# Performance work log

Measured on AMD Instinct MI355X. Metric: run time of the kernel, lower is better.

The kernel has to match this reference:

```python
import jax, jax.numpy as jnp
import numpy as np

LN_EPS = 1e-3  # keras LayerNormalization default epsilon


def setup_inputs() -> dict:
    key = jax.random.key(0)
    ks = jax.random.split(key, 6)
    B, S, D, H, K = 4, 4096, 1024, 16, 64
    scale = 1.0 / np.sqrt(D)
    return {
        "x": jax.random.normal(ks[0], (B, S, D), jnp.float32),
        "Wq": jax.random.normal(ks[1], (D, H, K), jnp.float32) * scale,
        "bq": jnp.zeros((H, K), jnp.float32),
        "Wk": jax.random.normal(ks[2], (D, H, K), jnp.float32) * scale,
        "bk": jnp.zeros((H, K), jnp.float32),
        "Wv": jax.random.normal(ks[3], (D, H, K), jnp.float32) * scale,
        "bv": jnp.zeros((H, K), jnp.float32),
        "Wo": jax.random.normal(ks[4], (H, K, D), jnp.float32) * scale,
        "bo": jnp.zeros((D,), jnp.float32),
        "gamma": jnp.ones((D,), jnp.float32),
        "beta": jnp.zeros((D,), jnp.float32),
        "num_window": 8,
    }


def reference(x, Wq, bq, Wk, bk, Wv, bv, Wo, bo, gamma, beta, num_window):
    B, S, D = x.shape
    H, K = Wq.shape[1], Wq.shape[2]
    Sw = S // num_window
    # Block-diagonal (windowed) attention: reshape seq into windows instead of a Python loop.
    xw = x.reshape(B, num_window, Sw, D)  # [B, W, Sw, D]
    q = jnp.einsum('bwsd,dhk->bwshk', xw, Wq) + bq
    k = jnp.einsum('bwsd,dhk->bwshk', xw, Wk) + bk
    v = jnp.einsum('bwsd,dhk->bwshk', xw, Wv) + bv
    scores = jnp.einsum('bwqhk,bwshk->bwhqs', q, k) / jnp.sqrt(jnp.asarray(K, x.dtype))
    attn = jax.nn.softmax(scores, axis=-1)  # [B, W, H, Sw, Sw]
    ctx = jnp.einsum('bwhqs,bwshk->bwqhk', attn, v)
    attn_out = (jnp.einsum('bwqhk,hkd->bwqd', ctx, Wo) + bo).reshape(B, S, D)
    # residual + layernorm (keras eps=1e-3)
    y = x + attn_out
    mu = jnp.mean(y, axis=-1, keepdims=True)
    var = jnp.mean(jnp.square(y - mu), axis=-1, keepdims=True)
    return (y - mu) * jax.lax.rsqrt(var + LN_EPS) * gamma + beta
```

## Files before the change

### kernel.cpp

```cpp
#include <hip/hip_runtime.h>

typedef __bf16 bf16_t;
typedef __bf16 bf16x4 __attribute__((ext_vector_type(4)));
typedef __bf16 bf16x8 __attribute__((ext_vector_type(8)));
typedef float f32x4 __attribute__((ext_vector_type(4)));

#define MFMA16(a, b, c) __builtin_amdgcn_mfma_f32_16x16x32_bf16((a), (b), (c), 0, 0, 0)

__device__ __forceinline__ void gl_lds16(const bf16_t* g, bf16_t* l) {
  __builtin_amdgcn_global_load_lds(
      (const __attribute__((address_space(1))) void*)g,
      (__attribute__((address_space(3))) void*)l, 16, 0, 0);
}

__global__ __launch_bounds__(256) void cast_x_kernel(const float* __restrict__ x,
                                                     bf16_t* __restrict__ xb) {
  size_t i = (size_t)blockIdx.x * 256 + threadIdx.x;
  float4 v = ((const float4*)x)[i];
  bf16x4 o = {(bf16_t)v.x, (bf16_t)v.y, (bf16_t)v.z, (bf16_t)v.w};
  ((bf16x4*)xb)[i] = o;
}

__global__ __launch_bounds__(256) void transpose_w_kernel(
    const float* __restrict__ Wq, const float* __restrict__ Wk,
    const float* __restrict__ Wv, const float* __restrict__ Wo,
    bf16_t* __restrict__ Wt, bf16_t* __restrict__ WoT) {
  __shared__ bf16_t T[64 * 68];
  const int z = blockIdx.z;
  const float* src = (z == 0) ? Wq : (z == 1) ? Wk : (z == 2) ? Wv : Wo;
  bf16_t* dst = (z < 3) ? (Wt + (size_t)z * 1024 * 1024) : WoT;
  const int tr = blockIdx.y * 64;
  const int tc = blockIdx.x * 64;
  const int tid = threadIdx.x;
#pragma unroll
  for (int it = 0; it < 4; ++it) {
    int t = tid + it * 256;
    int row = t >> 4, c4 = t & 15;
    float4 v = *(const float4*)&src[(size_t)(tr + row) * 1024 + tc + c4 * 4];
    bf16x4 o = {(bf16_t)v.x, (bf16_t)v.y, (bf16_t)v.z, (bf16_t)v.w};
    *(bf16x4*)&T[row * 68 + c4 * 4] = o;
  }
  __syncthreads();
#pragma unroll
  for (int it = 0; it < 2; ++it) {
    int t = tid + it * 256;
    int n = t >> 3, d8 = t & 7;
    bf16x8 o;
#pragma unroll
    for (int j = 0; j < 8; ++j) o[j] = T[(d8 * 8 + j) * 68 + n];
    *(bf16x8*)&dst[(size_t)(tc + n) * 1024 + tr + d8 * 8] = o;
  }
}

__global__ __launch_bounds__(256) void gemm_qkv_kernel(
    const bf16_t* __restrict__ A, const bf16_t* __restrict__ Bt,
    const float* __restrict__ bq, const float* __restrict__ bk,
    const float* __restrict__ bv, bf16_t* __restrict__ C) {
  __shared__ bf16_t As[128 * 64];
  __shared__ bf16_t Bs[128 * 64];
  const int tid = threadIdx.x;
  const int bm = blockIdx.y, bn = blockIdx.x;
  const int quad = (tid >> 4) & 3, l15 = tid & 15;
  const int wv = tid >> 6;
  const int wm = (wv & 1) * 64, wn = (wv >> 1) * 64;

  f32x4 acc[4][4];
  f32x4 zero = {0.f, 0.f, 0.f, 0.f};
#pragma unroll
  for (int i = 0; i < 4; ++i)
#pragma unroll
    for (int j = 0; j < 4; ++j) acc[i][j] = zero;

  const bf16_t* Abase = A + (size_t)(bm * 128) * 1024;
  const bf16_t* Bbase = Bt + (size_t)(bn * 128) * 1024;

  for (int kt = 0; kt < 16; ++kt) {
    const int k0 = kt * 64;
#pragma unroll
    for (int i = 0; i < 4; ++i) {
      int t = tid + i * 256;
      int row = t >> 3;
      int g = (t & 7) ^ (row & 7);
      gl_lds16(Abase + (size_t)row * 1024 + k0 + g * 8, &As[t * 8]);
      gl_lds16(Bbase + (size_t)row * 1024 + k0 + g * 8, &Bs[t * 8]);
    }
    __syncthreads();
#pragma unroll
    for (int kh = 0; kh < 2; ++kh) {
      bf16x8 af[4], bfr[4];
#pragma unroll
      for (int mi = 0; mi < 4; ++mi) {
        int r = wm + mi * 16 + l15;
        af[mi] = *(const bf16x8*)&As[r * 64 + (((kh * 4 + quad) ^ (r & 7)) << 3)];
      }
#pragma unroll
      for (int ni = 0; ni < 4; ++ni) {
        int r = wn + ni * 16 + l15;
        bfr[ni] = *(const bf16x8*)&Bs[r * 64 + (((kh * 4 + quad) ^ (r & 7)) << 3)];
      }
#pragma unroll
      for (int mi = 0; mi < 4; ++mi)
#pragma unroll
        for (int ni = 0; ni < 4; ++ni)
          acc[mi][ni] = MFMA16(af[mi], bfr[ni], acc[mi][ni]);
    }
    __syncthreads();
  }

#pragma unroll
  for (int ni = 0; ni < 4; ++ni) {
    int col = bn * 128 + wn + ni * 16 + l15;
    float bias, scale;
    if (col < 1024) {
      bias = bq[col];
      scale = 0.125f;
    } else if (col < 2048) {
      bias = bk[col - 1024];
      scale = 1.f;
    } else {
      bias = bv[col - 2048];
      scale = 1.f;
    }
#pragma unroll
    for (int mi = 0; mi < 4; ++mi) {
      int row = bm * 128 + wm + mi * 16 + quad * 4;
#pragma unroll
      for (int r = 0; r < 4; ++r)
        C[(size_t)(row + r) * 3072 + col] = (bf16_t)((acc[mi][ni][r] + bias) * scale);
    }
  }
}

__global__ __launch_bounds__(256) void transpose_v_kernel(
    const bf16_t* __restrict__ QKV, bf16_t* __restrict__ Vt) {
  __shared__ bf16_t T[64 * 68];
  const int hid = blockIdx.x, sc = blockIdx.y;
  const int b = hid >> 7, w = (hid >> 4) & 7, h = hid & 15;
  const int rowb = b * 4096 + w * 512 + sc * 64;
  const bf16_t* src = QKV + (size_t)rowb * 3072 + 2048 + h * 64;
  const int tid = threadIdx.x;
#pragma unroll
  for (int it = 0; it < 2; ++it) {
    int t = tid + it * 256;
    int row = t >> 3, c8 = t & 7;
    bf16x8 v = *(const bf16x8*)&src[(size_t)row * 3072 + c8 * 8];
    bf16x4 lo = {v[0], v[1], v[2], v[3]};
    bf16x4 hi = {v[4], v[5], v[6], v[7]};
    *(bf16x4*)&T[row * 68 + c8 * 8] = lo;
    *(bf16x4*)&T[row * 68 + c8 * 8 + 4] = hi;
  }
  __syncthreads();
#pragma unroll
  for (int it = 0; it < 2; ++it) {
    int t = tid + it * 256;
    int n = t >> 3, d8 = t & 7;
    bf16x8 o;
#pragma unroll
    for (int j = 0; j < 8; ++j) o[j] = T[(d8 * 8 + j) * 68 + n];
    *(bf16x8*)&Vt[((size_t)hid * 64 + n) * 512 + sc * 64 + d8 * 8] = o;
  }
}

__global__ __launch_bounds__(256) void attn_kernel(
    const bf16_t* __restrict__ QKV, const bf16_t* __restrict__ Vt,
    bf16_t* __restrict__ Ctx) {
  __shared__ bf16_t Ks[64 * 64];
  __shared__ bf16_t Vs[64 * 64];
  __shared__ bf16_t Pb[4][16 * 64];

  const int tid = threadIdx.x;
  const int wv = tid >> 6, quad = (tid >> 4) & 3, l15 = tid & 15;
  const int hid = blockIdx.x, qb = blockIdx.y;
  const int b = hid >> 7, w = (hid >> 4) & 7, h = hid & 15;
  const int rowQ = b * 4096 + w * 512 + qb * 64 + wv * 16 + l15;
  const int krow0 = b * 4096 + w * 512;

  bf16x8 qf[2];
#pragma unroll
  for (int kh = 0; kh < 2; ++kh)
    qf[kh] = *(const bf16x8*)&QKV[(size_t)rowQ * 3072 + h * 64 + kh * 32 + quad * 8];

  const bf16_t* Kb = QKV + (size_t)krow0 * 3072 + 1024 + h * 64;
  const bf16_t* Vb = Vt + (size_t)hid * 64 * 512;

  float lp[4] = {0.f, 0.f, 0.f, 0.f};
  f32x4 Oa[4];
  f32x4 zero = {0.f, 0.f, 0.f, 0.f};
#pragma unroll
  for (int dt = 0; dt < 4; ++dt) Oa[dt] = zero;

  for (int kt = 0; kt < 8; ++kt) {
#pragma unroll
    for (int i = 0; i < 2; ++i) {
      int t = tid + i * 256;
      int row = t >> 3;
      int g = (t & 7) ^ (row & 7);
      gl_lds16(Kb + (size_t)(kt * 64 + row) * 3072 + g * 8, &Ks[t * 8]);
      gl_lds16(Vb + (size_t)row * 512 + kt * 64 + g * 8, &Vs[t * 8]);
    }
    __syncthreads();

    f32x4 s[4];
#pragma unroll
    for (int jt = 0; jt < 4; ++jt) {
      f32x4 a = zero;
#pragma unroll
      for (int kh = 0; kh < 2; ++kh) {
        int key = jt * 16 + l15;
        bf16x8 kf = *(const bf16x8*)&Ks[key * 64 + (((kh * 4 + quad) ^ (key & 7)) << 3)];
        a = MFMA16(qf[kh], kf, a);
      }
      s[jt] = a;
    }

#pragma unroll
    for (int jt = 0; jt < 4; ++jt)
#pragma unroll
      for (int r = 0; r < 4; ++r) {
        float p = __expf(s[jt][r]);
        s[jt][r] = p;
        lp[r] += p;
      }

#pragma unroll
    for (int jt = 0; jt < 4; ++jt) {
#pragma unroll
      for (int r = 0; r < 4; ++r) {
        int prow = quad * 4 + r;
        int gcol = (jt * 2 + (l15 >> 3)) ^ (prow & 7);
        Pb[wv][prow * 64 + gcol * 8 + (l15 & 7)] = (bf16_t)s[jt][r];
      }
    }
#pragma unroll
    for (int kh = 0; kh < 2; ++kh) {
      bf16x8 pf = *(const bf16x8*)&Pb[wv][l15 * 64 + (((kh * 4 + quad) ^ (l15 & 7)) << 3)];
#pragma unroll
      for (int dt = 0; dt < 4; ++dt) {
        int d = dt * 16 + l15;
        bf16x8 vf = *(const bf16x8*)&Vs[d * 64 + (((kh * 4 + quad) ^ (d & 7)) << 3)];
        Oa[dt] = MFMA16(pf, vf, Oa[dt]);
      }
    }
    __syncthreads();
  }

  float inv[4];
#pragma unroll
  for (int r = 0; r < 4; ++r) {
    float rs = lp[r];
    rs += __shfl_xor(rs, 1, 64);
    rs += __shfl_xor(rs, 2, 64);
    rs += __shfl_xor(rs, 4, 64);
    rs += __shfl_xor(rs, 8, 64);
    inv[r] = 1.0f / rs;
  }

#pragma unroll
  for (int dt = 0; dt < 4; ++dt) {
#pragma unroll
    for (int r = 0; r < 4; ++r) {
      int orow = b * 4096 + w * 512 + qb * 64 + wv * 16 + quad * 4 + r;
      Ctx[(size_t)orow * 1024 + h * 64 + dt * 16 + l15] = (bf16_t)(Oa[dt][r] * inv[r]);
    }
  }
}

__global__ __launch_bounds__(256) void gemm_proj_kernel(
    const bf16_t* __restrict__ A, const bf16_t* __restrict__ Bt,
    const float* __restrict__ bo, const float* __restrict__ x,
    float* __restrict__ Y) {
  __shared__ bf16_t As[128 * 64];
  __shared__ bf16_t Bs[128 * 64];
  const int tid = threadIdx.x;
  const int bm = blockIdx.y, bn = blockIdx.x;
  const int quad = (tid >> 4) & 3, l15 = tid & 15;
  const int wv = tid >> 6;
  const int wm = (wv & 1) * 64, wn = (wv >> 1) * 64;

  f32x4 acc[4][4];
  f32x4 zero = {0.f, 0.f, 0.f, 0.f};
#pragma unroll
  for (int i = 0; i < 4; ++i)
#pragma unroll
    for (int j = 0; j < 4; ++j) acc[i][j] = zero;

  const bf16_t* Abase = A + (size_t)(bm * 128) * 1024;
  const bf16_t* Bbase = Bt + (size_t)(bn * 128) * 1024;

  for (int kt = 0; kt < 16; ++kt) {
    const int k0 = kt * 64;
#pragma unroll
    for (int i = 0; i < 4; ++i) {
      int t = tid + i * 256;
      int row = t >> 3;
      int g = (t & 7) ^ (row & 7);
      gl_lds16(Abase + (size_t)row * 1024 + k0 + g * 8, &As[t * 8]);
      gl_lds16(Bbase + (size_t)row * 1024 + k0 + g * 8, &Bs[t * 8]);
    }
    __syncthreads();
#pragma unroll
    for (int kh = 0; kh < 2; ++kh) {
      bf16x8 af[4], bfr[4];
#pragma unroll
      for (int mi = 0; mi < 4; ++mi) {
        int r = wm + mi * 16 + l15;
        af[mi] = *(const bf16x8*)&As[r * 64 + (((kh * 4 + quad) ^ (r & 7)) << 3)];
      }
#pragma unroll
      for (int ni = 0; ni < 4; ++ni) {
        int r = wn + ni * 16 + l15;
        bfr[ni] = *(const bf16x8*)&Bs[r * 64 + (((kh * 4 + quad) ^ (r & 7)) << 3)];
      }
#pragma unroll
      for (int mi = 0; mi < 4; ++mi)
#pragma unroll
        for (int ni = 0; ni < 4; ++ni)
          acc[mi][ni] = MFMA16(af[mi], bfr[ni], acc[mi][ni]);
    }
    __syncthreads();
  }

#pragma unroll
  for (int ni = 0; ni < 4; ++ni) {
    int col = bn * 128 + wn + ni * 16 + l15;
    float bias = bo[col];
#pragma unroll
    for (int mi = 0; mi < 4; ++mi) {
      int row = bm * 128 + wm + mi * 16 + quad * 4;
#pragma unroll
      for (int r = 0; r < 4; ++r) {
        size_t idx = (size_t)(row + r) * 1024 + col;
        Y[idx] = acc[mi][ni][r] + bias + x[idx];
      }
    }
  }
}

__global__ __launch_bounds__(256) void ln_kernel(float* __restrict__ Y,
                                                 const float* __restrict__ gamma,
                                                 const float* __restrict__ beta) {
  const int row = blockIdx.x, tid = threadIdx.x;
  float4 y = ((const float4*)(Y + (size_t)row * 1024))[tid];
  float s = y.x + y.y + y.z + y.w;
  float s2 = y.x * y.x + y.y * y.y + y.z * y.z + y.w * y.w;
#pragma unroll
  for (int off = 1; off < 64; off <<= 1) {
    s += __shfl_xor(s, off, 64);
    s2 += __shfl_xor(s2, off, 64);
  }
  __shared__ float red[8];
  int wv = tid >> 6;
  if ((tid & 63) == 0) {
    red[wv] = s;
    red[4 + wv] = s2;
  }
  __syncthreads();
  s = red[0] + red[1] + red[2] + red[3];
  s2 = red[4] + red[5] + red[6] + red[7];
  float mean = s * (1.0f / 1024.0f);
  float var = s2 * (1.0f / 1024.0f) - mean * mean;
  float rs = rsqrtf(var + 1e-3f);
  float4 g = ((const float4*)gamma)[tid];
  float4 bb = ((const float4*)beta)[tid];
  y.x = (y.x - mean) * rs * g.x + bb.x;
  y.y = (y.y - mean) * rs * g.y + bb.y;
  y.z = (y.z - mean) * rs * g.z + bb.z;
  y.w = (y.w - mean) * rs * g.w + bb.w;
  ((float4*)(Y + (size_t)row * 1024))[tid] = y;
}

extern "C" void kernel_launch(void* const* d_in, const int* in_sizes, int n_in,
                              void* d_out, int out_size, void* d_ws, size_t ws_size,
                              hipStream_t stream) {
  const float* x = (const float*)d_in[0];
  const float* Wq = (const float*)d_in[1];
  const float* bq = (const float*)d_in[2];
  const float* Wk = (const float*)d_in[3];
  const float* bk = (const float*)d_in[4];
  const float* Wv = (const float*)d_in[5];
  const float* bv = (const float*)d_in[6];
  const float* Wo = (const float*)d_in[7];
  const float* bo = (const float*)d_in[8];
  const float* gamma = (const float*)d_in[9];
  const float* beta = (const float*)d_in[10];
  float* Y = (float*)d_out;

  char* ws = (char*)d_ws;
  bf16_t* xb = (bf16_t*)(ws);
  bf16_t* Wt = (bf16_t*)(ws + 33554432);
  bf16_t* WoT = (bf16_t*)(ws + 39845888);
  bf16_t* QKVb = (bf16_t*)(ws + 41943040);
  bf16_t* Vtb = (bf16_t*)(ws + 142606336);
  bf16_t* Ctx = (bf16_t*)(ws + 176160768);

  cast_x_kernel<<<16384, 256, 0, stream>>>(x, xb);
  transpose_w_kernel<<<dim3(16, 16, 4), 256, 0, stream>>>(Wq, Wk, Wv, Wo, Wt, WoT);
  gemm_qkv_kernel<<<dim3(24, 128), 256, 0, stream>>>(xb, Wt, bq, bk, bv, QKVb);
  transpose_v_kernel<<<dim3(512, 8), 256, 0, stream>>>(QKVb, Vtb);
  attn_kernel<<<dim3(512, 8), 256, 0, stream>>>(QKVb, Vtb, Ctx);
  gemm_proj_kernel<<<dim3(8, 128), 256, 0, stream>>>(Ctx, WoT, bo, x, Y);
  ln_kernel<<<16384, 256, 0, stream>>>(Y, gamma, beta);
}
```

Baseline: 447.7 us.

## Fuse V transpose into attention and process two query tiles per wave

Removes the separate V-transpose kernel and its intermediate buffer: the attention kernel now loads V rows directly from the QKV buffer and scatters them transposed into a swizzled LDS tile. Each wave now handles 32 query rows (two 16-row tiles) instead of 16, so each K/V tile loaded into LDS is reused twice as much and the grid is halved. The cost is scalar element-wise LDS stores for V (possible bank conflicts), more registers per thread for the extra accumulators and hoisted K/V fragments, and fewer blocks.

```diff
diff --git a/kernel.cpp b/kernel.cpp
--- a/kernel.cpp
+++ b/kernel.cpp
@@ -131,39 +131,8 @@
   }
 }
 
-__global__ __launch_bounds__(256) void transpose_v_kernel(
-    const bf16_t* __restrict__ QKV, bf16_t* __restrict__ Vt) {
-  __shared__ bf16_t T[64 * 68];
-  const int hid = blockIdx.x, sc = blockIdx.y;
-  const int b = hid >> 7, w = (hid >> 4) & 7, h = hid & 15;
-  const int rowb = b * 4096 + w * 512 + sc * 64;
-  const bf16_t* src = QKV + (size_t)rowb * 3072 + 2048 + h * 64;
-  const int tid = threadIdx.x;
-#pragma unroll
-  for (int it = 0; it < 2; ++it) {
-    int t = tid + it * 256;
-    int row = t >> 3, c8 = t & 7;
-    bf16x8 v = *(const bf16x8*)&src[(size_t)row * 3072 + c8 * 8];
-    bf16x4 lo = {v[0], v[1], v[2], v[3]};
-    bf16x4 hi = {v[4], v[5], v[6], v[7]};
-    *(bf16x4*)&T[row * 68 + c8 * 8] = lo;
-    *(bf16x4*)&T[row * 68 + c8 * 8 + 4] = hi;
-  }
-  __syncthreads();
-#pragma unroll
-  for (int it = 0; it < 2; ++it) {
-    int t = tid + it * 256;
-    int n = t >> 3, d8 = t & 7;
-    bf16x8 o;
-#pragma unroll
-    for (int j = 0; j < 8; ++j) o[j] = T[(d8 * 8 + j) * 68 + n];
-    *(bf16x8*)&Vt[((size_t)hid * 64 + n) * 512 + sc * 64 + d8 * 8] = o;
-  }
-}
-
 __global__ __launch_bounds__(256) void attn_kernel(
-    const bf16_t* __restrict__ QKV, const bf16_t* __restrict__ Vt,
-    bf16_t* __restrict__ Ctx) {
+    const bf16_t* __restrict__ QKV, bf16_t* __restrict__ Ctx) {
   __shared__ bf16_t Ks[64 * 64];
   __shared__ bf16_t Vs[64 * 64];
   __shared__ bf16_t Pb[4][16 * 64];
@@ -172,22 +141,31 @@
   const int wv = tid >> 6, quad = (tid >> 4) & 3, l15 = tid & 15;
   const int hid = blockIdx.x, qb = blockIdx.y;
   const int b = hid >> 7, w = (hid >> 4) & 7, h = hid & 15;
-  const int rowQ = b * 4096 + w * 512 + qb * 64 + wv * 16 + l15;
-  const int krow0 = b * 4096 + w * 512;
-
-  bf16x8 qf[2];
-#pragma unroll
-  for (int kh = 0; kh < 2; ++kh)
-    qf[kh] = *(const bf16x8*)&QKV[(size_t)rowQ * 3072 + h * 64 + kh * 32 + quad * 8];
-
-  const bf16_t* Kb = QKV + (size_t)krow0 * 3072 + 1024 + h * 64;
-  const bf16_t* Vb = Vt + (size_t)hid * 64 * 512;
-
-  float lp[4] = {0.f, 0.f, 0.f, 0.f};
-  f32x4 Oa[4];
+  const int rowW = b * 4096 + w * 512;
+  const int qbase = qb * 128 + wv * 32;
+
+  bf16x8 qf[2][2];
+#pragma unroll
+  for (int qt = 0; qt < 2; ++qt) {
+    int rowQ = rowW + qbase + qt * 16 + l15;
+#pragma unroll
+    for (int kh = 0; kh < 2; ++kh)
+      qf[qt][kh] = *(const bf16x8*)&QKV[(size_t)rowQ * 3072 + h * 64 + kh * 32 + quad * 8];
+  }
+
+  const bf16_t* Kb = QKV + (size_t)rowW * 3072 + 1024 + h * 64;
+  const bf16_t* Vg = QKV + (size_t)rowW * 3072 + 2048 + h * 64;
+
+  float lp[2][4] = {{0.f, 0.f, 0.f, 0.f}, {0.f, 0.f, 0.f, 0.f}};
+  f32x4 Oa[2][4];
   f32x4 zero = {0.f, 0.f, 0.f, 0.f};
 #pragma unroll
-  for (int dt = 0; dt < 4; ++dt) Oa[dt] = zero;
+  for (int qt = 0; qt < 2; ++qt)
+#pragma unroll
+    for (int dt = 0; dt < 4; ++dt) Oa[qt][dt] = zero;
+
+  const int vrow = tid >> 2;
+  const int vseg = tid & 3;
 
   for (int kt = 0; kt < 8; ++kt) {
 #pragma unroll
@@ -196,72 +174,93 @@
       int row = t >> 3;
       int g = (t & 7) ^ (row & 7);
       gl_lds16(Kb + (size_t)(kt * 64 + row) * 3072 + g * 8, &Ks[t * 8]);
-      gl_lds16(Vb + (size_t)row * 512 + kt * 64 + g * 8, &Vs[t * 8]);
-    }
-    __syncthreads();
-
-    f32x4 s[4];
+    }
+    {
+      const bf16_t* src = Vg + (size_t)(kt * 64 + vrow) * 3072 + vseg * 16;
+      bf16x8 v0 = *(const bf16x8*)&src[0];
+      bf16x8 v1 = *(const bf16x8*)&src[8];
+      int sg = vrow >> 3, sr = vrow & 7;
+#pragma unroll
+      for (int j = 0; j < 8; ++j) {
+        int d0 = vseg * 16 + j;
+        Vs[d0 * 64 + ((sg ^ (d0 & 7)) << 3) + sr] = v0[j];
+        int d1 = vseg * 16 + 8 + j;
+        Vs[d1 * 64 + ((sg ^ (d1 & 7)) << 3) + sr] = v1[j];
+      }
+    }
+    __syncthreads();
+
+    bf16x8 kf[4][2], vf[2][4];
 #pragma unroll
     for (int jt = 0; jt < 4; ++jt) {
-      f32x4 a = zero;
-#pragma unroll
-      for (int kh = 0; kh < 2; ++kh) {
-        int key = jt * 16 + l15;
-        bf16x8 kf = *(const bf16x8*)&Ks[key * 64 + (((kh * 4 + quad) ^ (key & 7)) << 3)];
-        a = MFMA16(qf[kh], kf, a);
-      }
-      s[jt] = a;
-    }
-
-#pragma unroll
-    for (int jt = 0; jt < 4; ++jt)
-#pragma unroll
-      for (int r = 0; r < 4; ++r) {
-        float p = __expf(s[jt][r]);
-        s[jt][r] = p;
-        lp[r] += p;
-      }
-
-#pragma unroll
-    for (int jt = 0; jt < 4; ++jt) {
-#pragma unroll
-      for (int r = 0; r < 4; ++r) {
-        int prow = quad * 4 + r;
-        int gcol = (jt * 2 + (l15 >> 3)) ^ (prow & 7);
-        Pb[wv][prow * 64 + gcol * 8 + (l15 & 7)] = (bf16_t)s[jt][r];
-      }
-    }
-#pragma unroll
-    for (int kh = 0; kh < 2; ++kh) {
-      bf16x8 pf = *(const bf16x8*)&Pb[wv][l15 * 64 + (((kh * 4 + quad) ^ (l15 & 7)) << 3)];
+      int key = jt * 16 + l15;
+#pragma unroll
+      for (int kh = 0; kh < 2; ++kh)
+        kf[jt][kh] = *(const bf16x8*)&Ks[key * 64 + (((kh * 4 + quad) ^ (key & 7)) << 3)];
+    }
+#pragma unroll
+    for (int kh = 0; kh < 2; ++kh)
 #pragma unroll
       for (int dt = 0; dt < 4; ++dt) {
         int d = dt * 16 + l15;
-        bf16x8 vf = *(const bf16x8*)&Vs[d * 64 + (((kh * 4 + quad) ^ (d & 7)) << 3)];
-        Oa[dt] = MFMA16(pf, vf, Oa[dt]);
-      }
-    }
-    __syncthreads();
-  }
-
-  float inv[4];
-#pragma unroll
-  for (int r = 0; r < 4; ++r) {
-    float rs = lp[r];
-    rs += __shfl_xor(rs, 1, 64);
-    rs += __shfl_xor(rs, 2, 64);
-    rs += __shfl_xor(rs, 4, 64);
-    rs += __shfl_xor(rs, 8, 64);
-    inv[r] = 1.0f / rs;
-  }
-
-#pragma unroll
-  for (int dt = 0; dt < 4; ++dt) {
+        vf[kh][dt] = *(const bf16x8*)&Vs[d * 64 + (((kh * 4 + quad) ^ (d & 7)) << 3)];
+      }
+
+#pragma unroll
+    for (int qt = 0; qt < 2; ++qt) {
+      f32x4 s[4];
+#pragma unroll
+      for (int jt = 0; jt < 4; ++jt) {
+        f32x4 a = zero;
+#pragma unroll
+        for (int kh = 0; kh < 2; ++kh) a = MFMA16(qf[qt][kh], kf[jt][kh], a);
+        s[jt] = a;
+      }
+#pragma unroll
+      for (int jt = 0; jt < 4; ++jt)
+#pragma unroll
+        for (int r = 0; r < 4; ++r) {
+          float p = __expf(s[jt][r]);
+          s[jt][r] = p;
+          lp[qt][r] += p;
+        }
+#pragma unroll
+      for (int jt = 0; jt < 4; ++jt)
+#pragma unroll
+        for (int r = 0; r < 4; ++r) {
+          int prow = quad * 4 + r;
+          int gcol = (jt * 2 + (l15 >> 3)) ^ (prow & 7);
+          Pb[wv][prow * 64 + gcol * 8 + (l15 & 7)] = (bf16_t)s[jt][r];
+        }
+#pragma unroll
+      for (int kh = 0; kh < 2; ++kh) {
+        bf16x8 pf = *(const bf16x8*)&Pb[wv][l15 * 64 + (((kh * 4 + quad) ^ (l15 & 7)) << 3)];
+#pragma unroll
+        for (int dt = 0; dt < 4; ++dt) Oa[qt][dt] = MFMA16(pf, vf[kh][dt], Oa[qt][dt]);
+      }
+    }
+    __syncthreads();
+  }
+
+#pragma unroll
+  for (int qt = 0; qt < 2; ++qt) {
+    float inv[4];
 #pragma unroll
     for (int r = 0; r < 4; ++r) {
-      int orow = b * 4096 + w * 512 + qb * 64 + wv * 16 + quad * 4 + r;
-      Ctx[(size_t)orow * 1024 + h * 64 + dt * 16 + l15] = (bf16_t)(Oa[dt][r] * inv[r]);
-    }
+      float rs = lp[qt][r];
+      rs += __shfl_xor(rs, 1, 64);
+      rs += __shfl_xor(rs, 2, 64);
+      rs += __shfl_xor(rs, 4, 64);
+      rs += __shfl_xor(rs, 8, 64);
+      inv[r] = 1.0f / rs;
+    }
+#pragma unroll
+    for (int dt = 0; dt < 4; ++dt)
+#pragma unroll
+      for (int r = 0; r < 4; ++r) {
+        int orow = rowW + qbase + qt * 16 + quad * 4 + r;
+        Ctx[(size_t)orow * 1024 + h * 64 + dt * 16 + l15] = (bf16_t)(Oa[qt][dt][r] * inv[r]);
+      }
   }
 }
 
@@ -390,14 +389,12 @@
   bf16_t* Wt = (bf16_t*)(ws + 33554432);
   bf16_t* WoT = (bf16_t*)(ws + 39845888);
   bf16_t* QKVb = (bf16_t*)(ws + 41943040);
-  bf16_t* Vtb = (bf16_t*)(ws + 142606336);
-  bf16_t* Ctx = (bf16_t*)(ws + 176160768);
+  bf16_t* Ctx = (bf16_t*)(ws + 142606336);
 
   cast_x_kernel<<<16384, 256, 0, stream>>>(x, xb);
   transpose_w_kernel<<<dim3(16, 16, 4), 256, 0, stream>>>(Wq, Wk, Wv, Wo, Wt, WoT);
   gemm_qkv_kernel<<<dim3(24, 128), 256, 0, stream>>>(xb, Wt, bq, bk, bv, QKVb);
-  transpose_v_kernel<<<dim3(512, 8), 256, 0, stream>>>(QKVb, Vtb);
-  attn_kernel<<<dim3(512, 8), 256, 0, stream>>>(QKVb, Vtb, Ctx);
+  attn_kernel<<<dim3(512, 4), 256, 0, stream>>>(QKVb, Ctx);
   gemm_proj_kernel<<<dim3(8, 128), 256, 0, stream>>>(Ctx, WoT, bo, x, Y);
   ln_kernel<<<16384, 256, 0, stream>>>(Y, gamma, beta);
 }
```

Result: faster. 434.9 us (-2.9%).
